# Performance work log

Measured on AMD Instinct MI355X. Metric: run time of the kernel, lower is better.

Reference implementation:

```python
import jax, jax.numpy as jnp
import numpy as np

HEADS = 8  # head_num from init_kwargs


def setup_inputs() -> dict:
    key = jax.random.key(0)
    k1, k2, k3 = jax.random.split(key, 3)
    x = jax.random.normal(k1, (1, 512, 16, 16, 16), dtype=jnp.float32)
    # 1x1x1 Conv3d kernels are pointwise linear maps over channels
    w_qkv = jax.random.normal(k2, (1536, 512), dtype=jnp.float32) * 0.02
    w_out = jax.random.normal(k3, (512, 512), dtype=jnp.float32) * 0.02
    return {"x": x, "w_qkv": w_qkv, "w_out": w_out}


def reference(x, w_qkv, w_out):
    B, C, D, H, W = x.shape
    h = HEADS
    dh = C // h
    scale = float(dh) ** 0.5  # NOTE: source MULTIPLIES by sqrt(dh) (dk), faithful here
    N = D * H * W

    # pointwise Conv3d == per-token linear: [B, N, C]
    xt = x.reshape(B, C, N).transpose(0, 2, 1)
    qkv = xt @ w_qkv.T                                   # [B, N, 3C]
    qkv = qkv.reshape(B, N, 3, h, dh).transpose(2, 0, 3, 1, 4)  # [3, B, h, N, dh]
    q, k, v = qkv[0], qkv[1], qkv[2]

    energy = jnp.einsum('bhid,bhjd->bhij', q, k) * scale  # [B, h, N, N]
    attn = jax.nn.softmax(energy, axis=-1)
    o = jnp.einsum('bhij,bhjd->bhid', attn, v)            # [B, h, N, dh]

    o = o.transpose(0, 2, 1, 3).reshape(B, N, C)          # [B, N, C]
    out = o @ w_out.T                                     # [B, N, C]
    return out.transpose(0, 2, 1).reshape(B, C, D, H, W)
```

## Files before the change

kernel.cpp:

```cpp
#include <hip/hip_runtime.h>

typedef unsigned short u16;
typedef unsigned int u32;
typedef unsigned long long u64;
typedef __bf16 bf16x8 __attribute__((ext_vector_type(8)));
typedef float f32x4 __attribute__((ext_vector_type(4)));
typedef u16 u16x8 __attribute__((ext_vector_type(8)));

#define C_DIM 512
#define N_TOK 4096
#define HEADS 8
#define K3 1536
#define QSCALE 11.5415603071f

__device__ __forceinline__ u16 f2bf(float f) {
  u32 u = __builtin_bit_cast(u32, f);
  u += 0x7FFFu + ((u >> 16) & 1u);
  return (u16)(u >> 16);
}
__device__ __forceinline__ float bf2f(u16 b) {
  u32 u = ((u32)b) << 16;
  return __builtin_bit_cast(float, u);
}

__global__ void prep_w_kernel(const float* __restrict__ w, u16* __restrict__ A1) {
  int i = blockIdx.x * 256 + threadIdx.x;
  if (i >= 1536 * 512) return;
  int m = i >> 9, c = i & 511;
  float v = w[i];
  u16 hi = f2bf(v);
  u16 lo = f2bf(v - bf2f(hi));
  u16* row = A1 + (size_t)m * K3;
  row[c] = hi; row[512 + c] = hi; row[1024 + c] = lo;
}

__global__ void prep_wout_kernel(const float* __restrict__ w, u16* __restrict__ A2) {
  int i = blockIdx.x * 256 + threadIdx.x;
  if (i >= 512 * 512) return;
  A2[i] = f2bf(w[i]);
}

__global__ __launch_bounds__(256) void prep_x_kernel(const float* __restrict__ x, u16* __restrict__ B1) {
  __shared__ float lds[64][65];
  int n0 = blockIdx.x * 64, c0 = blockIdx.y * 64;
  int tid = threadIdx.x;
#pragma unroll
  for (int i = 0; i < 4; i++) {
    int idx = tid + i * 256;
    int r = idx >> 4, s = idx & 15;
    const float4 v = *(const float4*)(x + (size_t)(c0 + r) * N_TOK + n0 + s * 4);
    lds[r][s * 4 + 0] = v.x; lds[r][s * 4 + 1] = v.y;
    lds[r][s * 4 + 2] = v.z; lds[r][s * 4 + 3] = v.w;
  }
  __syncthreads();
  int n = tid >> 2, cs = tid & 3;
  u16x8 hv[2], lv[2];
#pragma unroll
  for (int half = 0; half < 2; half++) {
#pragma unroll
    for (int j = 0; j < 8; j++) {
      float v = lds[cs * 16 + half * 8 + j][n];
      u16 hi = f2bf(v);
      hv[half][j] = hi;
      lv[half][j] = f2bf(v - bf2f(hi));
    }
  }
  u16* row = B1 + (size_t)(n0 + n) * K3 + c0 + cs * 16;
  *(u16x8*)(row) = hv[0];
  *(u16x8*)(row + 8) = hv[1];
  *(u16x8*)(row + 512) = lv[0];
  *(u16x8*)(row + 520) = lv[1];
  *(u16x8*)(row + 1024) = hv[0];
  *(u16x8*)(row + 1032) = hv[1];
}

__global__ __launch_bounds__(256) void gemm_nt_kernel(
    const u16* __restrict__ A, const u16* __restrict__ B, float* __restrict__ C,
    int M, int N, int K) {
  __shared__ char lds[128 * 64 * 2 * 2];
  char* ldsA = lds;
  char* ldsB = lds + 128 * 64 * 2;
  int n0 = blockIdx.x * 128, m0 = blockIdx.y * 128;
  int tid = threadIdx.x, lane = tid & 63, wid = tid >> 6;
  int wr = wid >> 1, wc = wid & 1;
  f32x4 acc[4][4] = {};
  for (int k0 = 0; k0 < K; k0 += 64) {
    __syncthreads();
#pragma unroll
    for (int i = 0; i < 4; i++) {
      int idx = tid + i * 256;
      int row = idx >> 3, cb = idx & 7;
      uint4 va = *(const uint4*)(A + (size_t)(m0 + row) * K + k0 + cb * 8);
      *(uint4*)(ldsA + row * 128 + ((cb * 16) ^ ((row & 7) << 4))) = va;
      uint4 vb = *(const uint4*)(B + (size_t)(n0 + row) * K + k0 + cb * 8);
      *(uint4*)(ldsB + row * 128 + ((cb * 16) ^ ((row & 7) << 4))) = vb;
    }
    __syncthreads();
#pragma unroll
    for (int kk = 0; kk < 2; kk++) {
      bf16x8 af[4], bfr[4];
#pragma unroll
      for (int mt = 0; mt < 4; mt++) {
        int row = wr * 64 + mt * 16 + (lane & 15);
        int kb = kk * 64 + ((lane >> 4) << 4);
        af[mt] = *(const bf16x8*)(ldsA + row * 128 + (kb ^ ((row & 7) << 4)));
      }
#pragma unroll
      for (int nt = 0; nt < 4; nt++) {
        int row = wc * 64 + nt * 16 + (lane & 15);
        int kb = kk * 64 + ((lane >> 4) << 4);
        bfr[nt] = *(const bf16x8*)(ldsB + row * 128 + (kb ^ ((row & 7) << 4)));
      }
#pragma unroll
      for (int mt = 0; mt < 4; mt++)
#pragma unroll
        for (int nt = 0; nt < 4; nt++)
          acc[mt][nt] = __builtin_amdgcn_mfma_f32_16x16x32_bf16(af[mt], bfr[nt], acc[mt][nt], 0, 0, 0);
    }
  }
#pragma unroll
  for (int mt = 0; mt < 4; mt++)
#pragma unroll
    for (int nt = 0; nt < 4; nt++) {
      int row = m0 + wr * 64 + mt * 16 + ((lane >> 4) << 2);
      int col = n0 + wc * 64 + nt * 16 + (lane & 15);
#pragma unroll
      for (int r = 0; r < 4; r++)
        C[(size_t)(row + r) * N + col] = acc[mt][nt][r];
    }
}

__global__ void prep_qk_kernel(const float* __restrict__ qkv, u16* __restrict__ Qp, u16* __restrict__ Kp) {
  int i = blockIdx.x * 256 + threadIdx.x;
  int dh = i & 63;
  int n = (i >> 6) & 4095;
  int h = i >> 18;
  float q = qkv[(size_t)n * K3 + h * 64 + dh] * QSCALE;
  float k = qkv[(size_t)n * K3 + 512 + h * 64 + dh];
  u16 qhi = f2bf(q); u16 qlo = f2bf(q - bf2f(qhi));
  u16 khi = f2bf(k); u16 klo = f2bf(k - bf2f(khi));
  u16* qr = Qp + ((size_t)h * N_TOK + n) * 128;
  u16* kr = Kp + ((size_t)h * N_TOK + n) * 128;
  qr[dh] = qhi; qr[64 + dh] = qlo;
  kr[dh] = khi; kr[64 + dh] = klo;
}

__global__ __launch_bounds__(256) void prep_v_kernel(const float* __restrict__ qkv, u16* __restrict__ Vt) {
  __shared__ float lds[64][65];
  int n0 = blockIdx.x * 64, h = blockIdx.y;
  int tid = threadIdx.x;
#pragma unroll
  for (int i = 0; i < 4; i++) {
    int idx = tid + i * 256;
    int r = idx >> 4, s = idx & 15;
    const float4 v = *(const float4*)(qkv + (size_t)(n0 + r) * K3 + 1024 + h * 64 + s * 4);
    lds[r][s * 4 + 0] = v.x; lds[r][s * 4 + 1] = v.y;
    lds[r][s * 4 + 2] = v.z; lds[r][s * 4 + 3] = v.w;
  }
  __syncthreads();
  int dh = tid >> 2, ns = tid & 3;
  u16x8 pv[2];
#pragma unroll
  for (int half = 0; half < 2; half++)
#pragma unroll
    for (int j = 0; j < 8; j++)
      pv[half][j] = f2bf(lds[ns * 16 + half * 8 + j][dh]);
  u16* dst = Vt + ((size_t)h * 64 + dh) * N_TOK + n0 + ns * 16;
  *(u16x8*)(dst) = pv[0];
  *(u16x8*)(dst + 8) = pv[1];
}

__global__ __launch_bounds__(256) void attn_kernel(
    const u16* __restrict__ Qp, const u16* __restrict__ Kp,
    const u16* __restrict__ Vt, float* __restrict__ Uws,
    float* __restrict__ Mws, float* __restrict__ Lws) {
  __shared__ char lds[32768];
  char* ldsK = lds;
  char* ldsV = lds + 16384;
  char* ldsP = lds + 24576;
  int bid = blockIdx.x;
  int h = bid & 7;
  int rest = bid >> 3;
  int half = rest & 1;
  int q0 = (rest >> 1) * 64;
  int kvbase = half * 2048;
  int tid = threadIdx.x, lane = tid & 63, wid = tid >> 6;
  char* myP = ldsP + wid * 2048;
  int qcol = lane & 15;
  int g = lane >> 4;

  bf16x8 qf[4];
  {
    const u16* qrow = Qp + ((size_t)h * N_TOK + q0 + wid * 16 + qcol) * 128 + (g * 8);
#pragma unroll
    for (int c = 0; c < 4; c++) qf[c] = *(const bf16x8*)(qrow + c * 32);
  }
  const u16* Kbase = Kp + (size_t)h * N_TOK * 128;
  const u16* Vbase = Vt + (size_t)h * 64 * N_TOK;

  f32x4 o[4] = {};
  float mrow = -INFINITY, lrow = 0.f;

  for (int t = 0; t < 32; ++t) {
    int kv0 = kvbase + t * 64;
    __syncthreads();
#pragma unroll
    for (int i = 0; i < 4; i++) {
      int idx = tid + i * 256, row = idx >> 4, cb = idx & 15;
      uint4 v = *(const uint4*)(Kbase + (size_t)(kv0 + row) * 128 + cb * 8);
      *(uint4*)(ldsK + row * 256 + ((cb * 16) ^ ((row & 7) << 4))) = v;
    }
#pragma unroll
    for (int i = 0; i < 2; i++) {
      int idx = tid + i * 256, row = idx >> 3, cb = idx & 7;
      uint4 v = *(const uint4*)(Vbase + (size_t)row * N_TOK + kv0 + cb * 8);
      *(uint4*)(ldsV + row * 128 + ((cb * 16) ^ ((row & 7) << 4))) = v;
    }
    __syncthreads();

    f32x4 s[4];
#pragma unroll
    for (int nt = 0; nt < 4; nt++) {
      int row = nt * 16 + qcol;
      const char* kb = ldsK + row * 256;
      int swz = (row & 7) << 4;
      int ko = g << 4;
      bf16x8 kf0 = *(const bf16x8*)(kb + ((ko) ^ swz));
      bf16x8 kf1 = *(const bf16x8*)(kb + ((64 + ko) ^ swz));
      bf16x8 kf2 = *(const bf16x8*)(kb + ((128 + ko) ^ swz));
      bf16x8 kf3 = *(const bf16x8*)(kb + ((192 + ko) ^ swz));
      f32x4 acc = {};
      acc = __builtin_amdgcn_mfma_f32_16x16x32_bf16(kf0, qf[0], acc, 0, 0, 0);
      acc = __builtin_amdgcn_mfma_f32_16x16x32_bf16(kf1, qf[1], acc, 0, 0, 0);
      acc = __builtin_amdgcn_mfma_f32_16x16x32_bf16(kf2, qf[0], acc, 0, 0, 0);
      acc = __builtin_amdgcn_mfma_f32_16x16x32_bf16(kf3, qf[1], acc, 0, 0, 0);
      acc = __builtin_amdgcn_mfma_f32_16x16x32_bf16(kf0, qf[2], acc, 0, 0, 0);
      acc = __builtin_amdgcn_mfma_f32_16x16x32_bf16(kf1, qf[3], acc, 0, 0, 0);
      s[nt] = acc;
    }

    float m = s[0][0];
#pragma unroll
    for (int nt = 0; nt < 4; nt++)
#pragma unroll
      for (int r = 0; r < 4; r++) m = fmaxf(m, s[nt][r]);
    m = fmaxf(m, __shfl_xor(m, 16));
    m = fmaxf(m, __shfl_xor(m, 32));
    float mnew = fmaxf(mrow, m);
    float alpha = exp2f(mrow - mnew);
    mrow = mnew;
    float psum = 0.f;
#pragma unroll
    for (int nt = 0; nt < 4; nt++)
#pragma unroll
      for (int r = 0; r < 4; r++) {
        float p = exp2f(s[nt][r] - mnew);
        s[nt][r] = p;
        psum += p;
      }
    psum += __shfl_xor(psum, 16);
    psum += __shfl_xor(psum, 32);
    lrow = lrow * alpha + psum;

#pragma unroll
    for (int r = 0; r < 4; r++) {
      float a = __shfl(alpha, (g << 2) | r);
      o[0][r] *= a; o[1][r] *= a; o[2][r] *= a; o[3][r] *= a;
    }

#pragma unroll
    for (int nt = 0; nt < 4; nt++) {
      u16 h0 = f2bf(s[nt][0]), h1 = f2bf(s[nt][1]);
      u16 h2 = f2bf(s[nt][2]), h3 = f2bf(s[nt][3]);
      u32 w0 = (u32)h0 | ((u32)h1 << 16);
      u32 w1 = (u32)h2 | ((u32)h3 << 16);
      int off = (nt * 32 + g * 8) ^ ((qcol & 7) << 4);
      *(uint2*)(myP + qcol * 128 + off) = make_uint2(w0, w1);
    }

#pragma unroll
    for (int c = 0; c < 2; c++) {
      int prow = lane & 15;
      int kb2 = c * 64 + (g << 4);
      bf16x8 pf = *(const bf16x8*)(myP + prow * 128 + (kb2 ^ ((prow & 7) << 4)));
#pragma unroll
      for (int nt = 0; nt < 4; nt++) {
        int vrow = nt * 16 + (lane & 15);
        bf16x8 vf = *(const bf16x8*)(ldsV + vrow * 128 + (kb2 ^ ((vrow & 7) << 4)));
        o[nt] = __builtin_amdgcn_mfma_f32_16x16x32_bf16(pf, vf, o[nt], 0, 0, 0);
      }
    }
  }

  size_t base = ((size_t)(half * HEADS + h) * N_TOK);
#pragma unroll
  for (int r = 0; r < 4; r++) {
    int tok = q0 + wid * 16 + (g << 2) + r;
    float* urow = Uws + (base + tok) * 64;
#pragma unroll
    for (int nt = 0; nt < 4; nt++)
      urow[nt * 16 + (lane & 15)] = o[nt][r];
  }
  if (g == 0) {
    int tok = q0 + wid * 16 + qcol;
    Mws[base + tok] = mrow;
    Lws[base + tok] = lrow;
  }
}

__global__ void reduce_kernel(const float* __restrict__ Uws, const float* __restrict__ Mws,
                              const float* __restrict__ Lws, u16* __restrict__ Obuf) {
  int i = blockIdx.x * 256 + threadIdx.x;
  int d4 = i & 15;
  int tok = (i >> 4) & 4095;
  int h = i >> 16;
  size_t b1 = (size_t)h * N_TOK + tok;
  size_t b2 = (size_t)(HEADS + h) * N_TOK + tok;
  float m1 = Mws[b1], m2 = Mws[b2];
  float l1 = Lws[b1], l2 = Lws[b2];
  float m = fmaxf(m1, m2);
  float w1 = exp2f(m1 - m), w2 = exp2f(m2 - m);
  float inv = 1.0f / (l1 * w1 + l2 * w2);
  f32x4 u1 = *(const f32x4*)(Uws + b1 * 64 + d4 * 4);
  f32x4 u2 = *(const f32x4*)(Uws + b2 * 64 + d4 * 4);
  u16* dst = Obuf + (size_t)tok * C_DIM + h * 64 + d4 * 4;
#pragma unroll
  for (int j = 0; j < 4; j++)
    dst[j] = f2bf((u1[j] * w1 + u2[j] * w2) * inv);
}

extern "C" void kernel_launch(void* const* d_in, const int* in_sizes, int n_in,
                              void* d_out, int out_size, void* d_ws, size_t ws_size,
                              hipStream_t stream) {
  const float* x = (const float*)d_in[0];
  const float* w_qkv = (const float*)d_in[1];
  const float* w_out = (const float*)d_in[2];
  float* out = (float*)d_out;
  char* ws = (char*)d_ws;
  size_t off = 0;
  size_t off_B1 = off;  off += (size_t)N_TOK * K3 * 2;
  size_t off_A1 = off;  off += (size_t)K3 * K3 * 2;
  size_t off_A2 = off;  off += (size_t)512 * 512 * 2;
  size_t off_qkv = off; off += (size_t)N_TOK * K3 * 4;
  size_t off_Qp = off;  off += (size_t)HEADS * N_TOK * 128 * 2;
  size_t off_Kp = off;  off += (size_t)HEADS * N_TOK * 128 * 2;
  u16* B1 = (u16*)(ws + off_B1);
  u16* A1 = (u16*)(ws + off_A1);
  u16* A2 = (u16*)(ws + off_A2);
  float* qkv = (float*)(ws + off_qkv);
  u16* Qp = (u16*)(ws + off_Qp);
  u16* Kp = (u16*)(ws + off_Kp);
  u16* Vt = (u16*)(ws + off_A1);
  u16* Obuf = (u16*)(ws + off_B1);
  float* Uws = (float*)(ws + off_qkv);
  float* Mws = (float*)(ws + off_qkv + 16777216);
  float* Lws = (float*)(ws + off_qkv + 16777216 + 262144);

  prep_w_kernel<<<(1536 * 512 + 255) / 256, 256, 0, stream>>>(w_qkv, A1);
  prep_wout_kernel<<<(512 * 512 + 255) / 256, 256, 0, stream>>>(w_out, A2);
  prep_x_kernel<<<dim3(64, 8), 256, 0, stream>>>(x, B1);
  gemm_nt_kernel<<<dim3(K3 / 128, N_TOK / 128), 256, 0, stream>>>(B1, A1, qkv, N_TOK, K3, K3);
  prep_qk_kernel<<<(HEADS * N_TOK * 64) / 256, 256, 0, stream>>>(qkv, Qp, Kp);
  prep_v_kernel<<<dim3(64, 8), 256, 0, stream>>>(qkv, Vt);
  attn_kernel<<<1024, 256, 0, stream>>>(Qp, Kp, Vt, Uws, Mws, Lws);
  reduce_kernel<<<(HEADS * N_TOK * 16) / 256, 256, 0, stream>>>(Uws, Mws, Lws, Obuf);
  gemm_nt_kernel<<<dim3(N_TOK / 128, 512 / 128), 256, 0, stream>>>(A2, Obuf, out, 512, N_TOK, 512);
}
```

Before: 235.5 us.

## Pre-swizzle GEMM operand images, use direct global-to-LDS loads, lazy softmax rescale

The prep kernels now write x and w_qkv as pre-swizzled 128x64 tile images, so a new GEMM kernel can fill LDS with global_load_lds without staging through registers. The attention loop gains several changes: the running-max rescale is skipped unless some row's max grows by more than 12, exp2 uses the raw v_exp_f32 instruction, P is converted with the native bf16 cast, and the MFMA sections are wrapped in s_setprio raises. These target global load latency, VALU cost of rescaling, and exp overhead. In exchange the layout becomes tied to fixed tile sizes, and the lazy rescale plus the approximate exp slightly change numerics.

```diff
diff --git a/kernel.cpp b/kernel.cpp
--- a/kernel.cpp
+++ b/kernel.cpp
@@ -2,8 +2,8 @@
 
 typedef unsigned short u16;
 typedef unsigned int u32;
-typedef unsigned long long u64;
 typedef __bf16 bf16x8 __attribute__((ext_vector_type(8)));
+typedef __bf16 bf16x4 __attribute__((ext_vector_type(4)));
 typedef float f32x4 __attribute__((ext_vector_type(4)));
 typedef u16 u16x8 __attribute__((ext_vector_type(8)));
 
@@ -13,6 +13,11 @@
 #define K3 1536
 #define QSCALE 11.5415603071f
 
+#define GLDS(SRC, DST)                                                        \
+  __builtin_amdgcn_global_load_lds(                                           \
+      (const __attribute__((address_space(1))) void*)(SRC),                   \
+      (__attribute__((address_space(3))) void*)(DST), 16, 0, 0)
+
 __device__ __forceinline__ u16 f2bf(float f) {
   u32 u = __builtin_bit_cast(u32, f);
   u += 0x7FFFu + ((u >> 16) & 1u);
@@ -22,16 +27,25 @@
   u32 u = ((u32)b) << 16;
   return __builtin_bit_cast(float, u);
 }
-
-__global__ void prep_w_kernel(const float* __restrict__ w, u16* __restrict__ A1) {
+__device__ __forceinline__ float fast_exp2(float x) {
+  float r;
+  asm("v_exp_f32 %0, %1" : "=v"(r) : "v"(x));
+  return r;
+}
+
+__global__ void prep_w_kernel(const float* __restrict__ w, u16* __restrict__ A1img) {
   int i = blockIdx.x * 256 + threadIdx.x;
   if (i >= 1536 * 512) return;
   int m = i >> 9, c = i & 511;
   float v = w[i];
   u16 hi = f2bf(v);
   u16 lo = f2bf(v - bf2f(hi));
-  u16* row = A1 + (size_t)m * K3;
-  row[c] = hi; row[512 + c] = hi; row[1024 + c] = lo;
+  int rr = m & 127, mb = m >> 7;
+  int kc = c & 63, kb0 = c >> 6;
+  int idx = (rr * 128 + (((kc >> 3) * 16) ^ ((rr & 7) << 4))) / 2 + (kc & 7);
+  A1img[((size_t)(mb * 24 + kb0)) * 8192 + idx] = hi;
+  A1img[((size_t)(mb * 24 + 8 + kb0)) * 8192 + idx] = hi;
+  A1img[((size_t)(mb * 24 + 16 + kb0)) * 8192 + idx] = lo;
 }
 
 __global__ void prep_wout_kernel(const float* __restrict__ w, u16* __restrict__ A2) {
@@ -40,7 +54,7 @@
   A2[i] = f2bf(w[i]);
 }
 
-__global__ __launch_bounds__(256) void prep_x_kernel(const float* __restrict__ x, u16* __restrict__ B1) {
+__global__ __launch_bounds__(256) void prep_x_kernel(const float* __restrict__ x, u16* __restrict__ B1img) {
   __shared__ float lds[64][65];
   int n0 = blockIdx.x * 64, c0 = blockIdx.y * 64;
   int tid = threadIdx.x;
@@ -53,25 +67,83 @@
     lds[r][s * 4 + 2] = v.z; lds[r][s * 4 + 3] = v.w;
   }
   __syncthreads();
-  int n = tid >> 2, cs = tid & 3;
-  u16x8 hv[2], lv[2];
-#pragma unroll
-  for (int half = 0; half < 2; half++) {
+  int n = n0 + (tid >> 2), cs = tid & 3;
+  int rr = n & 127, nb = n >> 7;
+  int kb0 = c0 >> 6;
+#pragma unroll
+  for (int half2 = 0; half2 < 2; half2++) {
+    u16x8 hv, lv;
 #pragma unroll
     for (int j = 0; j < 8; j++) {
-      float v = lds[cs * 16 + half * 8 + j][n];
+      float v = lds[cs * 16 + half2 * 8 + j][(tid >> 2)];
       u16 hi = f2bf(v);
-      hv[half][j] = hi;
-      lv[half][j] = f2bf(v - bf2f(hi));
-    }
-  }
-  u16* row = B1 + (size_t)(n0 + n) * K3 + c0 + cs * 16;
-  *(u16x8*)(row) = hv[0];
-  *(u16x8*)(row + 8) = hv[1];
-  *(u16x8*)(row + 512) = lv[0];
-  *(u16x8*)(row + 520) = lv[1];
-  *(u16x8*)(row + 1024) = hv[0];
-  *(u16x8*)(row + 1032) = hv[1];
+      hv[j] = hi;
+      lv[j] = f2bf(v - bf2f(hi));
+    }
+    int kc = cs * 16 + half2 * 8;
+    int idx = (rr * 128 + (((kc >> 3) * 16) ^ ((rr & 7) << 4))) / 2;
+    *(u16x8*)(B1img + ((size_t)(nb * 24 + kb0)) * 8192 + idx) = hv;
+    *(u16x8*)(B1img + ((size_t)(nb * 24 + 8 + kb0)) * 8192 + idx) = lv;
+    *(u16x8*)(B1img + ((size_t)(nb * 24 + 16 + kb0)) * 8192 + idx) = hv;
+  }
+}
+
+__global__ __launch_bounds__(256) void gemm_img_kernel(
+    const u16* __restrict__ Aimg, const u16* __restrict__ Bimg,
+    float* __restrict__ C, int M, int N, int K) {
+  __shared__ char lds[32768];
+  char* ldsA = lds;
+  char* ldsB = lds + 16384;
+  int n0 = blockIdx.x * 128, m0 = blockIdx.y * 128;
+  int nKb = K >> 6;
+  int tid = threadIdx.x, lane = tid & 63, wid = tid >> 6;
+  int wr = wid >> 1, wc = wid & 1;
+  const char* Abase = (const char*)Aimg + (size_t)blockIdx.y * nKb * 16384 + wid * 4096 + lane * 16;
+  const char* Bbase = (const char*)Bimg + (size_t)blockIdx.x * nKb * 16384 + wid * 4096 + lane * 16;
+  char* ldsAw = ldsA + wid * 4096;
+  char* ldsBw = ldsB + wid * 4096;
+  f32x4 acc[4][4] = {};
+  for (int kt = 0; kt < nKb; kt++) {
+    __syncthreads();
+    const char* a = Abase + (size_t)kt * 16384;
+    const char* b = Bbase + (size_t)kt * 16384;
+#pragma unroll
+    for (int j = 0; j < 4; j++) GLDS(a + j * 1024, ldsAw + j * 1024);
+#pragma unroll
+    for (int j = 0; j < 4; j++) GLDS(b + j * 1024, ldsBw + j * 1024);
+    __syncthreads();
+#pragma unroll
+    for (int kk = 0; kk < 2; kk++) {
+      bf16x8 af[4], bfr[4];
+#pragma unroll
+      for (int mt = 0; mt < 4; mt++) {
+        int row = wr * 64 + mt * 16 + (lane & 15);
+        int kb = kk * 64 + ((lane >> 4) << 4);
+        af[mt] = *(const bf16x8*)(ldsA + row * 128 + (kb ^ ((row & 7) << 4)));
+      }
+#pragma unroll
+      for (int nt = 0; nt < 4; nt++) {
+        int row = wc * 64 + nt * 16 + (lane & 15);
+        int kb = kk * 64 + ((lane >> 4) << 4);
+        bfr[nt] = *(const bf16x8*)(ldsB + row * 128 + (kb ^ ((row & 7) << 4)));
+      }
+#pragma unroll
+      for (int mt = 0; mt < 4; mt++)
+#pragma unroll
+        for (int nt = 0; nt < 4; nt++)
+          acc[mt][nt] = __builtin_amdgcn_mfma_f32_16x16x32_bf16(af[mt], bfr[nt], acc[mt][nt], 0, 0, 0);
+    }
+  }
+#pragma unroll
+  for (int mt = 0; mt < 4; mt++)
+#pragma unroll
+    for (int nt = 0; nt < 4; nt++) {
+      int row = m0 + wr * 64 + mt * 16 + ((lane >> 4) << 2);
+      int col = n0 + wc * 64 + nt * 16 + (lane & 15);
+#pragma unroll
+      for (int r = 0; r < 4; r++)
+        C[(size_t)(row + r) * N + col] = acc[mt][nt][r];
+    }
 }
 
 __global__ __launch_bounds__(256) void gemm_nt_kernel(
@@ -161,10 +233,10 @@
   int dh = tid >> 2, ns = tid & 3;
   u16x8 pv[2];
 #pragma unroll
-  for (int half = 0; half < 2; half++)
+  for (int half2 = 0; half2 < 2; half2++)
 #pragma unroll
     for (int j = 0; j < 8; j++)
-      pv[half][j] = f2bf(lds[ns * 16 + half * 8 + j][dh]);
+      pv[half2][j] = f2bf(lds[ns * 16 + half2 * 8 + j][dh]);
   u16* dst = Vt + ((size_t)h * 64 + dh) * N_TOK + n0 + ns * 16;
   *(u16x8*)(dst) = pv[0];
   *(u16x8*)(dst + 8) = pv[1];
@@ -219,6 +291,7 @@
     __syncthreads();
 
     f32x4 s[4];
+    __builtin_amdgcn_s_setprio(1);
 #pragma unroll
     for (int nt = 0; nt < 4; nt++) {
       int row = nt * 16 + qcol;
@@ -238,6 +311,7 @@
       acc = __builtin_amdgcn_mfma_f32_16x16x32_bf16(kf1, qf[3], acc, 0, 0, 0);
       s[nt] = acc;
     }
+    __builtin_amdgcn_s_setprio(0);
 
     float m = s[0][0];
 #pragma unroll
@@ -246,38 +320,40 @@
       for (int r = 0; r < 4; r++) m = fmaxf(m, s[nt][r]);
     m = fmaxf(m, __shfl_xor(m, 16));
     m = fmaxf(m, __shfl_xor(m, 32));
-    float mnew = fmaxf(mrow, m);
-    float alpha = exp2f(mrow - mnew);
-    mrow = mnew;
+    if (!__all(m - mrow <= 12.0f)) {
+      float mnew = fmaxf(mrow, m);
+      float alpha = fast_exp2(mrow - mnew);
+      mrow = mnew;
+      lrow *= alpha;
+#pragma unroll
+      for (int r = 0; r < 4; r++) {
+        float a = __shfl(alpha, (g << 2) | r);
+        o[0][r] *= a; o[1][r] *= a; o[2][r] *= a; o[3][r] *= a;
+      }
+    }
     float psum = 0.f;
 #pragma unroll
     for (int nt = 0; nt < 4; nt++)
 #pragma unroll
       for (int r = 0; r < 4; r++) {
-        float p = exp2f(s[nt][r] - mnew);
+        float p = fast_exp2(s[nt][r] - mrow);
         s[nt][r] = p;
         psum += p;
       }
     psum += __shfl_xor(psum, 16);
     psum += __shfl_xor(psum, 32);
-    lrow = lrow * alpha + psum;
-
-#pragma unroll
-    for (int r = 0; r < 4; r++) {
-      float a = __shfl(alpha, (g << 2) | r);
-      o[0][r] *= a; o[1][r] *= a; o[2][r] *= a; o[3][r] *= a;
-    }
+    lrow += psum;
 
 #pragma unroll
     for (int nt = 0; nt < 4; nt++) {
-      u16 h0 = f2bf(s[nt][0]), h1 = f2bf(s[nt][1]);
-      u16 h2 = f2bf(s[nt][2]), h3 = f2bf(s[nt][3]);
-      u32 w0 = (u32)h0 | ((u32)h1 << 16);
-      u32 w1 = (u32)h2 | ((u32)h3 << 16);
+      bf16x4 pb;
+      pb[0] = (__bf16)s[nt][0]; pb[1] = (__bf16)s[nt][1];
+      pb[2] = (__bf16)s[nt][2]; pb[3] = (__bf16)s[nt][3];
       int off = (nt * 32 + g * 8) ^ ((qcol & 7) << 4);
-      *(uint2*)(myP + qcol * 128 + off) = make_uint2(w0, w1);
-    }
-
+      *(bf16x4*)(myP + qcol * 128 + off) = pb;
+    }
+
+    __builtin_amdgcn_s_setprio(1);
 #pragma unroll
     for (int c = 0; c < 2; c++) {
       int prow = lane & 15;
@@ -290,6 +366,7 @@
         o[nt] = __builtin_amdgcn_mfma_f32_16x16x32_bf16(pf, vf, o[nt], 0, 0, 0);
       }
     }
+    __builtin_amdgcn_s_setprio(0);
   }
 
   size_t base = ((size_t)(half * HEADS + h) * N_TOK);
@@ -344,8 +421,8 @@
   size_t off_qkv = off; off += (size_t)N_TOK * K3 * 4;
   size_t off_Qp = off;  off += (size_t)HEADS * N_TOK * 128 * 2;
   size_t off_Kp = off;  off += (size_t)HEADS * N_TOK * 128 * 2;
-  u16* B1 = (u16*)(ws + off_B1);
-  u16* A1 = (u16*)(ws + off_A1);
+  u16* B1img = (u16*)(ws + off_B1);
+  u16* A1img = (u16*)(ws + off_A1);
   u16* A2 = (u16*)(ws + off_A2);
   float* qkv = (float*)(ws + off_qkv);
   u16* Qp = (u16*)(ws + off_Qp);
@@ -356,10 +433,10 @@
   float* Mws = (float*)(ws + off_qkv + 16777216);
   float* Lws = (float*)(ws + off_qkv + 16777216 + 262144);
 
-  prep_w_kernel<<<(1536 * 512 + 255) / 256, 256, 0, stream>>>(w_qkv, A1);
+  prep_w_kernel<<<(1536 * 512 + 255) / 256, 256, 0, stream>>>(w_qkv, A1img);
   prep_wout_kernel<<<(512 * 512 + 255) / 256, 256, 0, stream>>>(w_out, A2);
-  prep_x_kernel<<<dim3(64, 8), 256, 0, stream>>>(x, B1);
-  gemm_nt_kernel<<<dim3(K3 / 128, N_TOK / 128), 256, 0, stream>>>(B1, A1, qkv, N_TOK, K3, K3);
+  prep_x_kernel<<<dim3(64, 8), 256, 0, stream>>>(x, B1img);
+  gemm_img_kernel<<<dim3(K3 / 128, N_TOK / 128), 256, 0, stream>>>(B1img, A1img, qkv, N_TOK, K3, K3);
   prep_qk_kernel<<<(HEADS * N_TOK * 64) / 256, 256, 0, stream>>>(qkv, Qp, Kp);
   prep_v_kernel<<<dim3(64, 8), 256, 0, stream>>>(qkv, Vt);
   attn_kernel<<<1024, 256, 0, stream>>>(Qp, Kp, Vt, Uws, Mws, Lws);
```

New measurement: 223.3 us. 1.05x faster.
